# Kernel optimization log

Hardware: AMD Instinct MI355X
Metric: run time of the kernel (lower is better)

Reference implementation:

```python
import jax, jax.numpy as jnp
import numpy as np

N_BOOKS = 8
TAU_Q = 5.0

def setup_inputs() -> dict:
    key = jax.random.key(0)
    k1, k2, k3 = jax.random.split(key, 3)
    N, D_in = 65536, 512
    D = 512          # N_books * L_word
    N_words = 256
    x = jax.random.normal(k1, (N, D_in), dtype=jnp.float32)
    # xavier-uniform-like scale for fc weight [D_out, D_in]
    lim_w = float(np.sqrt(6.0 / (D_in + D)))
    W = jax.random.uniform(k2, (D, D_in), dtype=jnp.float32, minval=-lim_w, maxval=lim_w)
    b = jnp.zeros((D,), dtype=jnp.float32)
    lim_c = float(np.sqrt(6.0 / (N_words + D)))
    C = jax.random.uniform(k3, (N_words, D), dtype=jnp.float32, minval=-lim_c, maxval=lim_c)
    return {"x": x, "W": W, "b": b, "C": C}

def reference(x, W, b, C):
    # fc: X = x @ W^T + b  -> [N, D]
    X = x @ W.T + b
    N, D = X.shape
    M = C.shape[0]
    L = D // N_BOOKS
    Xb = X.reshape(N, N_BOOKS, L)          # [N, B, L]
    Cb = C.reshape(M, N_BOOKS, L)          # [M, B, L]
    x2 = jnp.sum(Xb * Xb, axis=-1)[:, :, None]           # [N, B, 1]
    c2 = jnp.sum(Cb * Cb, axis=-1).T[None, :, :]         # [1, B, M]
    xc = jnp.einsum('nbl,mbl->nbm', Xb, Cb)              # [N, B, M]
    dist = x2 + c2 - 2.0 * xc
    soft = jax.nn.softmax(-TAU_Q * dist, axis=-1)        # softmax over codewords
    # weighted codebook sum per book, then concat books -> [N, D]
    Z = jnp.einsum('nbm,mbl->nbl', soft, Cb).reshape(N, D)
    return X, Z
```

## Files before the change

### kernel.cpp

```cpp
#include <hip/hip_runtime.h>
#include <cstdint>
#include <cstddef>

#define N_ROWS   65536
#define D_IN     512
#define D_OUT    512
#define N_WORDS  256
#define N_BOOKS  8
#define TAU      5.0f
#define LOG2E    1.44269504088896340736f

typedef __attribute__((ext_vector_type(8))) short short8;
typedef __attribute__((ext_vector_type(4))) float f32x4;

__device__ __forceinline__ unsigned short f2bf(float f) {
    __bf16 h = (__bf16)f;
    return __builtin_bit_cast(unsigned short, h);
}
__device__ __forceinline__ float bf2f(unsigned short h) {
    unsigned u = ((unsigned)h) << 16;
    return __builtin_bit_cast(float, u);
}

__global__ __launch_bounds__(256) void prep_codebook(
        const float* __restrict__ C, const float* __restrict__ W,
        unsigned short* __restrict__ packA, unsigned short* __restrict__ packB,
        unsigned short* __restrict__ packW, float* __restrict__ nc2) {
    const int gid = blockIdx.x * 256 + threadIdx.x;
    if (gid < 131072) {
        const int i  = gid & 7;
        const int l  = (gid >> 3) & 63;
        const int mf = (gid >> 9) & 15;
        const int ks = (gid >> 13) & 1;
        const int b  = gid >> 14;
        const int row = (l & 15) + 16 * mf;
        const int col = b * 64 + (l >> 4) * 8 + i + 32 * ks;
        packA[gid] = f2bf(C[(size_t)row * D_IN + col]);
    } else if (gid < 262144) {
        const int g   = gid - 131072;
        const int i   = g & 7;
        const int l   = (g >> 3) & 63;
        const int n2  = (g >> 9) & 3;
        const int ks2 = (g >> 11) & 7;
        const int b   = g >> 14;
        const int m   = 32 * ks2 + 16 * (i >> 2) + 4 * (l >> 4) + (i & 3);
        const int col = b * 64 + n2 * 16 + (l & 15);
        packB[g] = f2bf(C[(size_t)m * D_IN + col]);
    } else if (gid < 524288) {
        const int h  = gid - 262144;
        const int i  = h & 7;
        const int l  = (h >> 3) & 63;
        const int cf = (h >> 9) & 7;
        const int kk = (h >> 12) & 15;
        const int bn = h >> 16;
        packW[h] = f2bf(W[(size_t)(bn * 128 + cf * 16 + (l & 15)) * D_IN
                          + kk * 32 + (l >> 4) * 8 + i]);
    } else if (gid < 526336) {
        const int t = gid - 524288;
        const int b = t >> 8, m = t & 255;
        const float* cp = C + (size_t)m * D_IN + b * 64;
        float s = 0.f;
        for (int l = 0; l < 64; ++l) {
            const float v = bf2f(f2bf(cp[l]));
            s = fmaf(v, v, s);
        }
        nc2[t] = -TAU * LOG2E * s;
    }
}

#define ASTR 40

__global__ __launch_bounds__(512, 4) void gemm_fc(
        const float* __restrict__ x, const unsigned short* __restrict__ packW,
        const float* __restrict__ bias, float* __restrict__ X) {
    __shared__ unsigned short Asm[2][256 * ASTR];
    __shared__ __attribute__((aligned(16))) unsigned short Wsm[2][4096];

    const int tid = threadIdx.x;
    const int bid = blockIdx.x;
    const int xcd = bid & 7;
    const int idx = bid >> 3;
    const int bm  = xcd * 32 + (idx >> 2);
    const int bn  = idx & 3;
    const int n0 = bm * 256, c0 = bn * 128;
    const int lane = tid & 63, w = tid >> 6;
    const int wr = w >> 1, wc = w & 1;
    const int lo = lane & 15, hi = lane >> 4;

    const int sr = tid >> 1;
    const int sf = (tid & 1) << 4;

    f32x4 acc[4][4];
    #pragma unroll
    for (int i = 0; i < 4; ++i)
        #pragma unroll
        for (int j = 0; j < 4; ++j) acc[i][j] = (f32x4){0.f, 0.f, 0.f, 0.f};

    const float4* gW = reinterpret_cast<const float4*>(packW);

    float4 ra[4];
    float4 rw;
    {
        const float* xa = &x[(size_t)(n0 + sr) * D_IN + sf];
        #pragma unroll
        for (int q = 0; q < 4; ++q)
            ra[q] = *reinterpret_cast<const float4*>(xa + q * 4);
        rw = gW[(size_t)(bn * 16) * 512 + tid];
    }
    #pragma unroll
    for (int q = 0; q < 4; ++q) {
        ushort4 pa;
        pa.x = f2bf(ra[q].x); pa.y = f2bf(ra[q].y);
        pa.z = f2bf(ra[q].z); pa.w = f2bf(ra[q].w);
        *reinterpret_cast<ushort4*>(&Asm[0][sr * ASTR + sf + q * 4]) = pa;
    }
    *reinterpret_cast<float4*>(&Wsm[0][tid * 8]) = rw;
    __syncthreads();

    for (int kk = 0; kk < 16; ++kk) {
        const int cur = kk & 1;
        if (kk < 15) {
            const float* xa = &x[(size_t)(n0 + sr) * D_IN + (kk + 1) * 32 + sf];
            #pragma unroll
            for (int q = 0; q < 4; ++q)
                ra[q] = *reinterpret_cast<const float4*>(xa + q * 4);
            rw = gW[(size_t)(bn * 16 + kk + 1) * 512 + tid];
        }
        short8 a[4], bb[4];
        #pragma unroll
        for (int fm = 0; fm < 4; ++fm)
            a[fm] = *reinterpret_cast<const short8*>(
                &Asm[cur][(wr * 64 + fm * 16 + lo) * ASTR + hi * 8]);
        #pragma unroll
        for (int cf = 0; cf < 4; ++cf)
            bb[cf] = *reinterpret_cast<const short8*>(
                &Wsm[cur][((wc * 4 + cf) * 64 + lane) * 8]);
        #pragma unroll
        for (int fm = 0; fm < 4; ++fm)
            #pragma unroll
            for (int cf = 0; cf < 4; ++cf)
                acc[fm][cf] = __builtin_amdgcn_mfma_f32_16x16x32_bf16(
                    a[fm], bb[cf], acc[fm][cf], 0, 0, 0);
        if (kk < 15) {
            #pragma unroll
            for (int q = 0; q < 4; ++q) {
                ushort4 pa;
                pa.x = f2bf(ra[q].x); pa.y = f2bf(ra[q].y);
                pa.z = f2bf(ra[q].z); pa.w = f2bf(ra[q].w);
                *reinterpret_cast<ushort4*>(&Asm[cur ^ 1][sr * ASTR + sf + q * 4]) = pa;
            }
            *reinterpret_cast<float4*>(&Wsm[cur ^ 1][tid * 8]) = rw;
            __syncthreads();
        }
    }

    #pragma unroll
    for (int cf = 0; cf < 4; ++cf) {
        const float bv = bias[c0 + wc * 64 + cf * 16 + lo];
        #pragma unroll
        for (int fm = 0; fm < 4; ++fm)
            #pragma unroll
            for (int j = 0; j < 4; ++j)
                X[(size_t)(n0 + wr * 64 + fm * 16 + hi * 4 + j) * D_OUT
                  + c0 + wc * 64 + cf * 16 + lo] = acc[fm][cf][j] + bv;
    }
}

__global__ __launch_bounds__(512, 4) void quant_head(
        const float* __restrict__ X, const unsigned short* __restrict__ packA,
        const unsigned short* __restrict__ packB, const float* __restrict__ nc2g,
        float* __restrict__ Z) {
    __shared__ __attribute__((aligned(16))) unsigned short cbA[16384];
    __shared__ __attribute__((aligned(16))) unsigned short cbB[16384];
    __shared__ float nc2s[256];

    const int tid  = threadIdx.x;
    const int bid  = blockIdx.x;
    const int xcd = bid & 7;
    const int idx = bid >> 3;
    const int b   = idx & 7;
    const int n0  = (xcd * 32 + (idx >> 3)) * 256;
    const int lane = tid & 63;
    const int w    = tid >> 6;
    const int lo = lane & 15, hi = lane >> 4;

    f32x4 rx[2][4];
    #pragma unroll
    for (int h = 0; h < 2; ++h) {
        const float* xp = X + (size_t)(n0 + w * 32 + h * 16 + lo) * D_OUT + b * 64 + hi * 8;
        rx[h][0] = __builtin_nontemporal_load(reinterpret_cast<const f32x4*>(xp));
        rx[h][1] = __builtin_nontemporal_load(reinterpret_cast<const f32x4*>(xp + 4));
        rx[h][2] = __builtin_nontemporal_load(reinterpret_cast<const f32x4*>(xp + 32));
        rx[h][3] = __builtin_nontemporal_load(reinterpret_cast<const f32x4*>(xp + 36));
    }

    {
        const float4* gA = reinterpret_cast<const float4*>(packA + (size_t)b * 16384);
        const float4* gB = reinterpret_cast<const float4*>(packB + (size_t)b * 16384);
        float4* sA = reinterpret_cast<float4*>(cbA);
        float4* sB = reinterpret_cast<float4*>(cbB);
        #pragma unroll
        for (int it = 0; it < 4; ++it) {
            sA[it * 512 + tid] = gA[it * 512 + tid];
            sB[it * 512 + tid] = gB[it * 512 + tid];
        }
        if (tid < 256) nc2s[tid] = nc2g[b * 256 + tid];
    }

    short8 xf[2][2];
    #pragma unroll
    for (int h = 0; h < 2; ++h)
        #pragma unroll
        for (int ks = 0; ks < 2; ++ks) {
            const f32x4 v0 = rx[h][ks * 2];
            const f32x4 v1 = rx[h][ks * 2 + 1];
            short8 t;
            t[0] = (short)f2bf(v0[0]); t[1] = (short)f2bf(v0[1]);
            t[2] = (short)f2bf(v0[2]); t[3] = (short)f2bf(v0[3]);
            t[4] = (short)f2bf(v1[0]); t[5] = (short)f2bf(v1[1]);
            t[6] = (short)f2bf(v1[2]); t[7] = (short)f2bf(v1[3]);
            xf[h][ks] = t;
        }

    __syncthreads();

    const float S2 = 2.0f * TAU * LOG2E;
    for (int h = 0; h < 2; ++h) {
        f32x4 qa[16];
        #pragma unroll
        for (int mf = 0; mf < 16; ++mf) qa[mf] = (f32x4){0.f, 0.f, 0.f, 0.f};
        #pragma unroll
        for (int ks = 0; ks < 2; ++ks)
            #pragma unroll
            for (int mf = 0; mf < 16; ++mf) {
                const short8 cfr = *reinterpret_cast<const short8*>(
                    &cbA[((ks * 16 + mf) * 64 + lane) * 8]);
                qa[mf] = __builtin_amdgcn_mfma_f32_16x16x32_bf16(
                    cfr, xf[h][ks], qa[mf], 0, 0, 0);
            }

        float s = 0.f;
        #pragma unroll
        for (int mf = 0; mf < 16; ++mf) {
            const f32x4 nv = *reinterpret_cast<const f32x4*>(&nc2s[mf * 16 + hi * 4]);
            const float p0 = exp2f(fmaf(qa[mf][0], S2, nv[0]));
            const float p1 = exp2f(fmaf(qa[mf][1], S2, nv[1]));
            const float p2 = exp2f(fmaf(qa[mf][2], S2, nv[2]));
            const float p3 = exp2f(fmaf(qa[mf][3], S2, nv[3]));
            qa[mf][0] = p0; qa[mf][1] = p1; qa[mf][2] = p2; qa[mf][3] = p3;
            s += (p0 + p1) + (p2 + p3);
        }
        s += __shfl_xor(s, 16, 64);
        s += __shfl_xor(s, 32, 64);
        const float inv = 1.0f / s;

        f32x4 acc2[4];
        #pragma unroll
        for (int n2 = 0; n2 < 4; ++n2) acc2[n2] = (f32x4){0.f, 0.f, 0.f, 0.f};
        #pragma unroll
        for (int ks2 = 0; ks2 < 8; ++ks2) {
            short8 pa;
            pa[0] = (short)f2bf(qa[2 * ks2][0]);     pa[1] = (short)f2bf(qa[2 * ks2][1]);
            pa[2] = (short)f2bf(qa[2 * ks2][2]);     pa[3] = (short)f2bf(qa[2 * ks2][3]);
            pa[4] = (short)f2bf(qa[2 * ks2 + 1][0]); pa[5] = (short)f2bf(qa[2 * ks2 + 1][1]);
            pa[6] = (short)f2bf(qa[2 * ks2 + 1][2]); pa[7] = (short)f2bf(qa[2 * ks2 + 1][3]);
            #pragma unroll
            for (int n2 = 0; n2 < 4; ++n2) {
                const short8 bv = *reinterpret_cast<const short8*>(
                    &cbB[((ks2 * 4 + n2) * 64 + lane) * 8]);
                acc2[n2] = __builtin_amdgcn_mfma_f32_16x16x32_bf16(pa, bv, acc2[n2], 0, 0, 0);
            }
        }

        float invr[4];
        #pragma unroll
        for (int j = 0; j < 4; ++j) invr[j] = __shfl(inv, hi * 4 + j, 64);
        #pragma unroll
        for (int n2 = 0; n2 < 4; ++n2)
            #pragma unroll
            for (int j = 0; j < 4; ++j)
                __builtin_nontemporal_store(
                    acc2[n2][j] * invr[j],
                    &Z[(size_t)(n0 + w * 32 + h * 16 + hi * 4 + j) * D_OUT
                       + b * 64 + n2 * 16 + lo]);
    }
}

extern "C" void kernel_launch(void* const* d_in, const int* in_sizes, int n_in,
                              void* d_out, int out_size, void* d_ws, size_t ws_size,
                              hipStream_t stream) {
    const float* x = (const float*)d_in[0];
    const float* W = (const float*)d_in[1];
    const float* b = (const float*)d_in[2];
    const float* C = (const float*)d_in[3];

    float* X = (float*)d_out;
    float* Z = X + (size_t)N_ROWS * D_OUT;

    unsigned short* packA = (unsigned short*)d_ws;
    unsigned short* packB = packA + 131072;
    unsigned short* packW = packB + 131072;
    float*          nc2g  = (float*)(packW + 262144);

    prep_codebook<<<dim3(2056), dim3(256), 0, stream>>>(C, W, packA, packB, packW, nc2g);
    gemm_fc<<<dim3(1024), dim3(512), 0, stream>>>(x, packW, b, X);
    quant_head<<<dim3(N_BOOKS * (N_ROWS / 256)), dim3(512), 0, stream>>>(
        X, packA, packB, nc2g, Z);
}
```

Measured before the change: 148.1 us.

## Interleave both row groups in quantizer MFMA loops to share codebook LDS loads

The quantizer kernel used to handle its two 16-row groups one after the other. It now processes both groups together, splitting the 256 codewords into two halves of 8 fragments. Each codebook fragment read from LDS now feeds two independent MFMAs, which halves LDS traffic and gives the matrix unit independent work to overlap. Softmax weights are packed to bf16 pairs right away, and the second GEMM also reuses each B fragment across both groups. This raises register pressure from the packed weights and the doubled accumulators, which may lower occupancy.

```diff
diff --git a/kernel.cpp b/kernel.cpp
--- a/kernel.cpp
+++ b/kernel.cpp
@@ -12,6 +12,7 @@
 
 typedef __attribute__((ext_vector_type(8))) short short8;
 typedef __attribute__((ext_vector_type(4))) float f32x4;
+typedef __attribute__((ext_vector_type(4))) unsigned uint4v;
 
 __device__ __forceinline__ unsigned short f2bf(float f) {
     __bf16 h = (__bf16)f;
@@ -186,12 +187,12 @@
 
     f32x4 rx[2][4];
     #pragma unroll
-    for (int h = 0; h < 2; ++h) {
-        const float* xp = X + (size_t)(n0 + w * 32 + h * 16 + lo) * D_OUT + b * 64 + hi * 8;
-        rx[h][0] = __builtin_nontemporal_load(reinterpret_cast<const f32x4*>(xp));
-        rx[h][1] = __builtin_nontemporal_load(reinterpret_cast<const f32x4*>(xp + 4));
-        rx[h][2] = __builtin_nontemporal_load(reinterpret_cast<const f32x4*>(xp + 32));
-        rx[h][3] = __builtin_nontemporal_load(reinterpret_cast<const f32x4*>(xp + 36));
+    for (int g = 0; g < 2; ++g) {
+        const float* xp = X + (size_t)(n0 + w * 32 + g * 16 + lo) * D_OUT + b * 64 + hi * 8;
+        rx[g][0] = __builtin_nontemporal_load(reinterpret_cast<const f32x4*>(xp));
+        rx[g][1] = __builtin_nontemporal_load(reinterpret_cast<const f32x4*>(xp + 4));
+        rx[g][2] = __builtin_nontemporal_load(reinterpret_cast<const f32x4*>(xp + 32));
+        rx[g][3] = __builtin_nontemporal_load(reinterpret_cast<const f32x4*>(xp + 36));
     }
 
     {
@@ -209,79 +210,105 @@
 
     short8 xf[2][2];
     #pragma unroll
-    for (int h = 0; h < 2; ++h)
+    for (int g = 0; g < 2; ++g)
         #pragma unroll
         for (int ks = 0; ks < 2; ++ks) {
-            const f32x4 v0 = rx[h][ks * 2];
-            const f32x4 v1 = rx[h][ks * 2 + 1];
+            const f32x4 v0 = rx[g][ks * 2];
+            const f32x4 v1 = rx[g][ks * 2 + 1];
             short8 t;
             t[0] = (short)f2bf(v0[0]); t[1] = (short)f2bf(v0[1]);
             t[2] = (short)f2bf(v0[2]); t[3] = (short)f2bf(v0[3]);
             t[4] = (short)f2bf(v1[0]); t[5] = (short)f2bf(v1[1]);
             t[6] = (short)f2bf(v1[2]); t[7] = (short)f2bf(v1[3]);
-            xf[h][ks] = t;
+            xf[g][ks] = t;
         }
 
     __syncthreads();
 
     const float S2 = 2.0f * TAU * LOG2E;
-    for (int h = 0; h < 2; ++h) {
-        f32x4 qa[16];
-        #pragma unroll
-        for (int mf = 0; mf < 16; ++mf) qa[mf] = (f32x4){0.f, 0.f, 0.f, 0.f};
+    float ssum[2] = {0.f, 0.f};
+    unsigned pk[2][2][16];
+
+    #pragma unroll
+    for (int H = 0; H < 2; ++H) {
+        f32x4 qa[2][8];
+        #pragma unroll
+        for (int g = 0; g < 2; ++g)
+            #pragma unroll
+            for (int mf = 0; mf < 8; ++mf) qa[g][mf] = (f32x4){0.f, 0.f, 0.f, 0.f};
         #pragma unroll
         for (int ks = 0; ks < 2; ++ks)
             #pragma unroll
-            for (int mf = 0; mf < 16; ++mf) {
+            for (int mf = 0; mf < 8; ++mf) {
                 const short8 cfr = *reinterpret_cast<const short8*>(
-                    &cbA[((ks * 16 + mf) * 64 + lane) * 8]);
-                qa[mf] = __builtin_amdgcn_mfma_f32_16x16x32_bf16(
-                    cfr, xf[h][ks], qa[mf], 0, 0, 0);
+                    &cbA[((ks * 16 + H * 8 + mf) * 64 + lane) * 8]);
+                qa[0][mf] = __builtin_amdgcn_mfma_f32_16x16x32_bf16(
+                    cfr, xf[0][ks], qa[0][mf], 0, 0, 0);
+                qa[1][mf] = __builtin_amdgcn_mfma_f32_16x16x32_bf16(
+                    cfr, xf[1][ks], qa[1][mf], 0, 0, 0);
             }
-
-        float s = 0.f;
-        #pragma unroll
-        for (int mf = 0; mf < 16; ++mf) {
-            const f32x4 nv = *reinterpret_cast<const f32x4*>(&nc2s[mf * 16 + hi * 4]);
-            const float p0 = exp2f(fmaf(qa[mf][0], S2, nv[0]));
-            const float p1 = exp2f(fmaf(qa[mf][1], S2, nv[1]));
-            const float p2 = exp2f(fmaf(qa[mf][2], S2, nv[2]));
-            const float p3 = exp2f(fmaf(qa[mf][3], S2, nv[3]));
-            qa[mf][0] = p0; qa[mf][1] = p1; qa[mf][2] = p2; qa[mf][3] = p3;
-            s += (p0 + p1) + (p2 + p3);
-        }
+        #pragma unroll
+        for (int mf = 0; mf < 8; ++mf) {
+            const f32x4 nv = *reinterpret_cast<const f32x4*>(
+                &nc2s[(H * 8 + mf) * 16 + hi * 4]);
+            #pragma unroll
+            for (int g = 0; g < 2; ++g) {
+                const float p0 = exp2f(fmaf(qa[g][mf][0], S2, nv[0]));
+                const float p1 = exp2f(fmaf(qa[g][mf][1], S2, nv[1]));
+                const float p2 = exp2f(fmaf(qa[g][mf][2], S2, nv[2]));
+                const float p3 = exp2f(fmaf(qa[g][mf][3], S2, nv[3]));
+                ssum[g] += (p0 + p1) + (p2 + p3);
+                pk[g][H][mf * 2]     = ((unsigned)f2bf(p1) << 16) | f2bf(p0);
+                pk[g][H][mf * 2 + 1] = ((unsigned)f2bf(p3) << 16) | f2bf(p2);
+            }
+        }
+    }
+
+    float inv[2];
+    #pragma unroll
+    for (int g = 0; g < 2; ++g) {
+        float s = ssum[g];
         s += __shfl_xor(s, 16, 64);
         s += __shfl_xor(s, 32, 64);
-        const float inv = 1.0f / s;
-
-        f32x4 acc2[4];
-        #pragma unroll
-        for (int n2 = 0; n2 < 4; ++n2) acc2[n2] = (f32x4){0.f, 0.f, 0.f, 0.f};
-        #pragma unroll
-        for (int ks2 = 0; ks2 < 8; ++ks2) {
-            short8 pa;
-            pa[0] = (short)f2bf(qa[2 * ks2][0]);     pa[1] = (short)f2bf(qa[2 * ks2][1]);
-            pa[2] = (short)f2bf(qa[2 * ks2][2]);     pa[3] = (short)f2bf(qa[2 * ks2][3]);
-            pa[4] = (short)f2bf(qa[2 * ks2 + 1][0]); pa[5] = (short)f2bf(qa[2 * ks2 + 1][1]);
-            pa[6] = (short)f2bf(qa[2 * ks2 + 1][2]); pa[7] = (short)f2bf(qa[2 * ks2 + 1][3]);
-            #pragma unroll
-            for (int n2 = 0; n2 < 4; ++n2) {
-                const short8 bv = *reinterpret_cast<const short8*>(
-                    &cbB[((ks2 * 4 + n2) * 64 + lane) * 8]);
-                acc2[n2] = __builtin_amdgcn_mfma_f32_16x16x32_bf16(pa, bv, acc2[n2], 0, 0, 0);
-            }
-        }
-
+        inv[g] = 1.0f / s;
+    }
+
+    f32x4 acc2[2][4];
+    #pragma unroll
+    for (int g = 0; g < 2; ++g)
+        #pragma unroll
+        for (int n2 = 0; n2 < 4; ++n2) acc2[g][n2] = (f32x4){0.f, 0.f, 0.f, 0.f};
+    #pragma unroll
+    for (int ks2 = 0; ks2 < 8; ++ks2) {
+        const int H  = ks2 >> 2;
+        const int sp = ks2 & 3;
+        const uint4v ua0 = {pk[0][H][4 * sp], pk[0][H][4 * sp + 1],
+                            pk[0][H][4 * sp + 2], pk[0][H][4 * sp + 3]};
+        const uint4v ua1 = {pk[1][H][4 * sp], pk[1][H][4 * sp + 1],
+                            pk[1][H][4 * sp + 2], pk[1][H][4 * sp + 3]};
+        const short8 pa0 = __builtin_bit_cast(short8, ua0);
+        const short8 pa1 = __builtin_bit_cast(short8, ua1);
+        #pragma unroll
+        for (int n2 = 0; n2 < 4; ++n2) {
+            const short8 bv = *reinterpret_cast<const short8*>(
+                &cbB[((ks2 * 4 + n2) * 64 + lane) * 8]);
+            acc2[0][n2] = __builtin_amdgcn_mfma_f32_16x16x32_bf16(pa0, bv, acc2[0][n2], 0, 0, 0);
+            acc2[1][n2] = __builtin_amdgcn_mfma_f32_16x16x32_bf16(pa1, bv, acc2[1][n2], 0, 0, 0);
+        }
+    }
+
+    #pragma unroll
+    for (int g = 0; g < 2; ++g) {
         float invr[4];
         #pragma unroll
-        for (int j = 0; j < 4; ++j) invr[j] = __shfl(inv, hi * 4 + j, 64);
+        for (int j = 0; j < 4; ++j) invr[j] = __shfl(inv[g], hi * 4 + j, 64);
         #pragma unroll
         for (int n2 = 0; n2 < 4; ++n2)
             #pragma unroll
             for (int j = 0; j < 4; ++j)
                 __builtin_nontemporal_store(
-                    acc2[n2][j] * invr[j],
-                    &Z[(size_t)(n0 + w * 32 + h * 16 + hi * 4 + j) * D_OUT
+                    acc2[g][n2][j] * invr[j],
+                    &Z[(size_t)(n0 + w * 32 + g * 16 + hi * 4 + j) * D_OUT
                        + b * 64 + n2 * 16 + lo]);
     }
 }
```

Result: no change. 148.7 us (+0.4%).
